# Performance work log

Hardware: AMD Instinct MI355X
Metric: run time of the kernel (lower is better)

Reference implementation:

```python
import jax, jax.numpy as jnp
import numpy as np

N_NODES = 100000
DEG = 16
N_EDGES = N_NODES * DEG
R = 8          # num_relations
C_IN = 64
C_OUT = 64


def setup_inputs() -> dict:
    key = jax.random.key(0)
    k1, k2, k3, k4 = jax.random.split(key, 4)
    x_feat = jax.random.normal(k1, (N_NODES, C_IN), dtype=jnp.float32)
    # xavier-ish scale for weight
    scale = (6.0 / (C_IN + C_OUT)) ** 0.5
    weight = jax.random.uniform(k2, (R + 1, C_IN, C_OUT), dtype=jnp.float32,
                                minval=-scale, maxval=scale)
    bias = jnp.zeros((C_OUT,), dtype=jnp.float32)
    # fixed-degree CSR: row_ptr = arange * DEG
    csr_row_ptr = (jnp.arange(N_NODES + 1, dtype=jnp.int64) * DEG)
    csr_col_ind = jax.random.randint(k3, (N_EDGES,), 0, N_NODES, dtype=jnp.int64)
    edge_type = jax.random.randint(k4, (N_EDGES,), 0, R, dtype=jnp.int64)
    return {"x_feat": x_feat, "weight": weight, "bias": bias,
            "csr_row_ptr": csr_row_ptr, "csr_col_ind": csr_col_ind,
            "edge_type": edge_type, "dup_count": DEG}


def reference(x_feat, weight, bias, csr_row_ptr, csr_col_ind, edge_type, dup_count):
    n_dst = csr_row_ptr.shape[0] - 1
    n_edges = csr_col_ind.shape[0]
    # per-edge destination node ids from CSR row pointer
    degrees = jnp.diff(csr_row_ptr)
    dst = jnp.repeat(jnp.arange(n_dst, dtype=csr_row_ptr.dtype), degrees,
                     total_repeat_length=n_edges)
    # segment id = (dst, relation) pair
    seg = (dst * R + edge_type).astype(jnp.int32)
    gathered = x_feat[csr_col_ind]                                  # [E, C_in]
    sums = jax.ops.segment_sum(gathered, seg, num_segments=n_dst * R)  # [N*R, C_in]
    counts = jax.ops.segment_sum(jnp.ones((n_edges,), x_feat.dtype), seg,
                                 num_segments=n_dst * R)
    # mean aggregation per (node, relation); empty relations -> 0
    agg = sums / jnp.maximum(counts, 1.0)[:, None]
    agg = agg.reshape(n_dst, R * x_feat.shape[1])                   # [N, R*C_in]
    # root (self) feature appended last, matching weight[-1]
    x_agg = jnp.concatenate([agg, x_feat[:n_dst]], axis=1)          # [N, (R+1)*C_in]
    y = x_agg @ weight.reshape(-1, weight.shape[-1]) + bias         # [N, C_out]
    return y
```

## Files before the change

kernel.cpp:

```cpp
#include <hip/hip_runtime.h>
#include <hip/hip_bf16.h>

#define R_REL   8
#define C_DIM   64
#define K_DIM   576
#define KT_N    18
#define CT_N    4
#define TILE_M  16
#define K_PAD   584

typedef __attribute__((ext_vector_type(8))) short bf16x8;
typedef __attribute__((ext_vector_type(4))) float f32x4;
typedef __attribute__((ext_vector_type(2))) unsigned u32x2;


static __device__ __forceinline__ unsigned short f2bf(float f) {
    union { float f; unsigned u; } v; v.f = f;
    unsigned r = v.u + 0x7FFFu + ((v.u >> 16) & 1u);
    return (unsigned short)(r >> 16);
}
static __device__ __forceinline__ float bf2f(unsigned u16) {
    union { unsigned u; float f; } v; v.u = u16 << 16;
    return v.f;
}

__global__ void pack_w_kernel(const float* __restrict__ w, unsigned int* __restrict__ wf) {
    int t = blockIdx.x * blockDim.x + threadIdx.x;
    if (t >= KT_N * CT_N * 64) return;
    int lane = t & 63;
    int ct   = (t >> 6) & 3;
    int kt   = t >> 8;
    int row0 = kt * 32 + (lane >> 4) * 8;
    int col  = ct * 16 + (lane & 15);
    unsigned short v[8];
#pragma unroll
    for (int j = 0; j < 8; ++j) {
        int rk = row0 + j;
        int wr = (rk < 512) ? rk : 512 + ((rk - 512) & 3) * 16 + ((rk - 512) >> 2);
        v[j] = f2bf(w[wr * C_DIM + col]);
    }
    uint4 o;
    o.x = (unsigned)v[0] | ((unsigned)v[1] << 16);
    o.y = (unsigned)v[2] | ((unsigned)v[3] << 16);
    o.z = (unsigned)v[4] | ((unsigned)v[5] << 16);
    o.w = (unsigned)v[6] | ((unsigned)v[7] << 16);
    ((uint4*)wf)[t] = o;
}

__global__ void cvt_x_kernel(const float* __restrict__ x, unsigned short* __restrict__ xb,
                             int total) {
    int t = blockIdx.x * blockDim.x + threadIdx.x;
    if (t >= total) return;
    int n = t >> 4, c = t & 15;
    const float* xr = x + (size_t)n * C_DIM + c;
    ushort4 o;
    o.x = f2bf(xr[0]);
    o.y = f2bf(xr[16]);
    o.z = f2bf(xr[32]);
    o.w = f2bf(xr[48]);
    *(ushort4*)(xb + (size_t)n * C_DIM + c * 4) = o;
}

#define ACCUM_SWITCH(RELV, VV)                                  \
    switch (RELV) {                                             \
        case 0: s0 += (VV); ++c0; break;                        \
        case 1: s1 += (VV); ++c1; break;                        \
        case 2: s2 += (VV); ++c2; break;                        \
        case 3: s3 += (VV); ++c3; break;                        \
        case 4: s4 += (VV); ++c4; break;                        \
        case 5: s5 += (VV); ++c5; break;                        \
        case 6: s6 += (VV); ++c6; break;                        \
        default: s7 += (VV); ++c7; break;                       \
    }

template<int USE_BF>
__global__ __launch_bounds__(256, 8) void rgcn_kernel(
    const float* __restrict__ x_feat,
    const unsigned short* __restrict__ xb,
    const float* __restrict__ bias,
    const int*   __restrict__ row_ptr,
    const int*   __restrict__ col_ind,
    const int*   __restrict__ edge_type,
    const unsigned short* __restrict__ wfrag,
    float* __restrict__ out,
    int n_nodes)
{
    __shared__ __align__(16) unsigned short xa[TILE_M][K_PAD];
    __shared__ __align__(16) int            col_lds[4][64];
    __shared__ __align__(8)  unsigned char  rel_lds[4][64];
    __shared__ __align__(4)  unsigned short inv_lds[4][32];

    const int tid   = threadIdx.x;
    const int lane  = tid & 63;
    const int w     = tid >> 6;
    const int m0    = blockIdx.x * TILE_M;
    const int nbase = m0 + w * 4;

    const int n_l   = nbase + (lane >> 4);
    const bool v_l  = n_l < n_nodes;
    int rp0   = v_l ? row_ptr[n_l]     : 0;
    int rp1   = v_l ? row_ptr[n_l + 1] : 0;
    int deg_l = v_l ? (rp1 - rp0) : -1;
    int col_l = col_ind[rp0 + (lane & 15)];
    int rel_l = edge_type[rp0 + (lane & 15)];

    const bool fast = USE_BF && (__ballot(deg_l == 16) == ~0ull);

    if (fast) {
        col_lds[w][lane] = col_l;
        rel_lds[w][lane] = (unsigned char)rel_l;
        unsigned long long bsel = 0;
#pragma unroll
        for (int r = 0; r < 8; ++r) {
            unsigned long long b = __ballot(rel_l == r);
            bsel = ((lane & 7) == r) ? b : bsel;
        }
        if (lane < 32) {
            int nd  = (lane >> 3) & 3;
            int cnt = __popcll(bsel & (0xFFFFull << (nd * 16)));
            inv_lds[w][lane] = f2bf(1.0f / (float)(cnt > 0 ? cnt : 1));
        }

        u32x2 selfv = *(const u32x2*)(xb + (size_t)(nbase + (lane >> 4)) * C_DIM
                                      + (lane & 15) * 4);
        *(u32x2*)&xa[w * 4 + (lane >> 4)][8 * C_DIM + (lane & 15) * 4] = selfv;

        const int q8 = (lane >> 4) * 8;
        int4 c0a = *(const int4*)&col_lds[w][q8];
        int4 c0b = *(const int4*)&col_lds[w][q8 + 4];
        int4 c1a = *(const int4*)&col_lds[w][32 + q8];
        int4 c1b = *(const int4*)&col_lds[w][32 + q8 + 4];
        int src0[8] = {c0a.x, c0a.y, c0a.z, c0a.w, c0b.x, c0b.y, c0b.z, c0b.w};
        int src1[8] = {c1a.x, c1a.y, c1a.z, c1a.w, c1b.x, c1b.y, c1b.z, c1b.w};

        const unsigned short* xbase = xb + (lane & 15) * 4;
        u32x2 gv0[8], gv1[8];
#pragma unroll
        for (int e = 0; e < 8; ++e) {
            gv0[e] = *(const u32x2*)(xbase + (size_t)src0[e] * C_DIM);
            gv1[e] = *(const u32x2*)(xbase + (size_t)src1[e] * C_DIM);
        }

        unsigned bw0[4][4], bw1[4][4];
#pragma unroll
        for (int d = 0; d < 4; ++d) {
            unsigned lx = gv0[2*d].x, hx = gv0[2*d+1].x;
            unsigned ly = gv0[2*d].y, hy = gv0[2*d+1].y;
            bw0[0][d] = (lx & 0xFFFFu) | (hx << 16);
            bw0[1][d] = (lx >> 16)     | (hx & 0xFFFF0000u);
            bw0[2][d] = (ly & 0xFFFFu) | (hy << 16);
            bw0[3][d] = (ly >> 16)     | (hy & 0xFFFF0000u);
            lx = gv1[2*d].x; hx = gv1[2*d+1].x;
            ly = gv1[2*d].y; hy = gv1[2*d+1].y;
            bw1[0][d] = (lx & 0xFFFFu) | (hx << 16);
            bw1[1][d] = (lx >> 16)     | (hx & 0xFFFF0000u);
            bw1[2][d] = (ly & 0xFFFFu) | (hy << 16);
            bw1[3][d] = (ly >> 16)     | (hy & 0xFFFF0000u);
        }

        const unsigned rl    = lane & 7;
        const bool     hi_ok = (lane >> 5) == ((lane & 15) >> 3);
#pragma unroll
        for (int pr = 0; pr < 2; ++pr) {
            const unsigned char* relp = &rel_lds[w][pr * 32 + q8];
            unsigned rlo = *(const unsigned*)relp;
            unsigned rhi = *(const unsigned*)(relp + 4);
            unsigned inv16 = inv_lds[w][(pr * 2 + ((lane & 15) >> 3)) * 8 + (lane & 7)];
            unsigned invg  = hi_ok ? inv16 : 0u;
            unsigned af[4];
#pragma unroll
            for (int d = 0; d < 4; ++d) {
                unsigned wrd = (d < 2) ? rlo : rhi;
                unsigned b0 = (wrd >> ((d & 1) * 16)) & 0xFFu;
                unsigned b1 = (wrd >> ((d & 1) * 16 + 8)) & 0xFFu;
                af[d] = (b0 == rl ? invg : 0u) | ((b1 == rl ? invg : 0u) << 16);
            }
            union { unsigned u[4]; bf16x8 v; } au;
            au.u[0] = af[0]; au.u[1] = af[1]; au.u[2] = af[2]; au.u[3] = af[3];

#pragma unroll
            for (int g = 0; g < 4; ++g) {
                union { unsigned u[4]; bf16x8 v; } bu;
                if (pr == 0) {
                    bu.u[0] = bw0[g][0]; bu.u[1] = bw0[g][1];
                    bu.u[2] = bw0[g][2]; bu.u[3] = bw0[g][3];
                } else {
                    bu.u[0] = bw1[g][0]; bu.u[1] = bw1[g][1];
                    bu.u[2] = bw1[g][2]; bu.u[3] = bw1[g][3];
                }
                f32x4 dacc = __builtin_amdgcn_mfma_f32_16x16x32_bf16(
                                 au.v, bu.v, (f32x4){0.f, 0.f, 0.f, 0.f}, 0, 0, 0);
#pragma unroll
                for (int reg = 0; reg < 4; ++reg) {
                    int m = (lane >> 4) * 4 + reg;
                    xa[w * 4 + pr * 2 + (m >> 3)][(m & 7) * C_DIM + g * 16 + (lane & 15)]
                        = f2bf(dacc[reg]);
                }
            }
        }
    } else {
        for (int mi_ = 0; mi_ < 4; ++mi_) {
            const int mi = w * 4 + mi_;
            const int n  = nbase + mi_;
            const int sdeg  = __builtin_amdgcn_readlane(deg_l, mi_ * 16);
            const int sbase = __builtin_amdgcn_readlane(rp0,   mi_ * 16);
            if (sdeg < 0) {
                for (int k = lane; k < K_DIM; k += 64) xa[mi][k] = 0;
                continue;
            }
            float s0=0,s1=0,s2=0,s3=0,s4=0,s5=0,s6=0,s7=0;
            int   c0=0,c1=0,c2=0,c3=0,c4=0,c5=0,c6=0,c7=0;
            const int ich = (lane & 15) * 4 + (lane >> 4);
            for (int e = 0; e < sdeg; ++e) {
                int src = col_ind[sbase + e];
                int rlv = edge_type[sbase + e];
                float vv = USE_BF ? bf2f(xb[(size_t)src * C_DIM + ich])
                                  : x_feat[(size_t)src * C_DIM + lane];
                ACCUM_SWITCH(rlv, vv)
            }
            xa[mi][0*C_DIM+lane] = f2bf(s0 * __fdividef(1.0f, (float)(c0>0?c0:1)));
            xa[mi][1*C_DIM+lane] = f2bf(s1 * __fdividef(1.0f, (float)(c1>0?c1:1)));
            xa[mi][2*C_DIM+lane] = f2bf(s2 * __fdividef(1.0f, (float)(c2>0?c2:1)));
            xa[mi][3*C_DIM+lane] = f2bf(s3 * __fdividef(1.0f, (float)(c3>0?c3:1)));
            xa[mi][4*C_DIM+lane] = f2bf(s4 * __fdividef(1.0f, (float)(c4>0?c4:1)));
            xa[mi][5*C_DIM+lane] = f2bf(s5 * __fdividef(1.0f, (float)(c5>0?c5:1)));
            xa[mi][6*C_DIM+lane] = f2bf(s6 * __fdividef(1.0f, (float)(c6>0?c6:1)));
            xa[mi][7*C_DIM+lane] = f2bf(s7 * __fdividef(1.0f, (float)(c7>0?c7:1)));
            xa[mi][8*C_DIM+lane] = USE_BF ? (unsigned short)xb[(size_t)n * C_DIM + lane]
                                          : f2bf(x_feat[(size_t)n * C_DIM
                                                        + (lane & 3) * 16 + (lane >> 2)]);
        }
    }
    __syncthreads();

    const int ct   = w;
    f32x4 acc = {0,0,0,0};
    const int arow = lane & 15;
    const int kgrp2 = lane >> 4;
    const bf16x8* wf8 = (const bf16x8*)wfrag;
#pragma unroll
    for (int kt = 0; kt < KT_N; ++kt) {
        bf16x8 a = *(const bf16x8*)&xa[arow][kt * 32 + kgrp2 * 8];
        acc = __builtin_amdgcn_mfma_f32_16x16x32_bf16(a, wf8[(kt*4 + ct)*64 + lane], acc, 0,0,0);
    }

    const int col   = ct * 16 + (lane & 15);
    const float b   = bias[col];
    const int rbase = (lane >> 4) * 4;
#pragma unroll
    for (int j = 0; j < 4; ++j) {
        int n = m0 + rbase + j;
        if (n < n_nodes)
            out[n * C_DIM + col] = acc[j] + b;
    }
}

extern "C" void kernel_launch(void* const* d_in, const int* in_sizes, int n_in,
                              void* d_out, int out_size, void* d_ws, size_t ws_size,
                              hipStream_t stream) {
    const float* x_feat    = (const float*)d_in[0];
    const float* weight    = (const float*)d_in[1];
    const float* bias      = (const float*)d_in[2];
    const int*   row_ptr   = (const int*)d_in[3];
    const int*   col_ind   = (const int*)d_in[4];
    const int*   edge_type = (const int*)d_in[5];
    float* out = (float*)d_out;

    const int n_nodes = in_sizes[3] - 1;
    const int nblocks = (n_nodes + TILE_M - 1) / TILE_M;

    unsigned int* wfrag = (unsigned int*)d_ws;
    const size_t wf_bytes = (size_t)KT_N * CT_N * 64 * 16;
    const size_t xb_bytes = (size_t)n_nodes * C_DIM * 2;

    pack_w_kernel<<<(KT_N * CT_N * 64 + 255) / 256, 256, 0, stream>>>(weight, wfrag);

    if (ws_size >= wf_bytes + xb_bytes) {
        unsigned short* xb = (unsigned short*)((char*)d_ws + wf_bytes);
        int total = n_nodes * 16;
        cvt_x_kernel<<<(total + 255) / 256, 256, 0, stream>>>(x_feat, xb, total);
        rgcn_kernel<1><<<nblocks, 256, 0, stream>>>(x_feat, xb, bias, row_ptr, col_ind,
                                                    edge_type, (const unsigned short*)d_ws,
                                                    out, n_nodes);
    } else {
        rgcn_kernel<0><<<nblocks, 256, 0, stream>>>(x_feat, nullptr, bias, row_ptr, col_ind,
                                                    edge_type, (const unsigned short*)d_ws,
                                                    out, n_nodes);
    }
}
```

Measured before the change: 56.44 us.

## Fuse weight pack and x conversion, use bpermute for columns, pack LDS writes

```diff
diff --git a/kernel.cpp b/kernel.cpp
--- a/kernel.cpp
+++ b/kernel.cpp
@@ -8,6 +8,7 @@
 #define CT_N    4
 #define TILE_M  16
 #define K_PAD   584
+#define PACK_T  (KT_N * CT_N * 64)
 
 typedef __attribute__((ext_vector_type(8))) short bf16x8;
 typedef __attribute__((ext_vector_type(4))) float f32x4;
@@ -24,34 +25,40 @@
     return v.f;
 }
 
-__global__ void pack_w_kernel(const float* __restrict__ w, unsigned int* __restrict__ wf) {
-    int t = blockIdx.x * blockDim.x + threadIdx.x;
-    if (t >= KT_N * CT_N * 64) return;
-    int lane = t & 63;
-    int ct   = (t >> 6) & 3;
-    int kt   = t >> 8;
-    int row0 = kt * 32 + (lane >> 4) * 8;
-    int col  = ct * 16 + (lane & 15);
-    unsigned short v[8];
-#pragma unroll
-    for (int j = 0; j < 8; ++j) {
-        int rk = row0 + j;
-        int wr = (rk < 512) ? rk : 512 + ((rk - 512) & 3) * 16 + ((rk - 512) >> 2);
-        v[j] = f2bf(w[wr * C_DIM + col]);
-    }
-    uint4 o;
-    o.x = (unsigned)v[0] | ((unsigned)v[1] << 16);
-    o.y = (unsigned)v[2] | ((unsigned)v[3] << 16);
-    o.z = (unsigned)v[4] | ((unsigned)v[5] << 16);
-    o.w = (unsigned)v[6] | ((unsigned)v[7] << 16);
-    ((uint4*)wf)[t] = o;
-}
-
-__global__ void cvt_x_kernel(const float* __restrict__ x, unsigned short* __restrict__ xb,
-                             int total) {
-    int t = blockIdx.x * blockDim.x + threadIdx.x;
-    if (t >= total) return;
-    int n = t >> 4, c = t & 15;
+__global__ void prep_kernel(const float* __restrict__ x, const float* __restrict__ wt,
+                            unsigned short* __restrict__ xb, unsigned int* __restrict__ wf,
+                            int total_cvt) {
+    int t = blockIdx.x * 256 + threadIdx.x;
+    if (t < PACK_T) {
+        int lane = t & 63;
+        int ct   = (t >> 6) & 3;
+        int kt   = t >> 8;
+        int row0 = kt * 32 + (lane >> 4) * 8;
+        int col  = ct * 16 + (lane & 15);
+        unsigned short v[8];
+#pragma unroll
+        for (int j = 0; j < 8; ++j) {
+            int rk = row0 + j;
+            int wr;
+            if (rk < 512) {
+                int rel = rk & 7, c = (rk >> 3) & 15, g = rk >> 7;
+                wr = rel * C_DIM + g * 16 + c;
+            } else {
+                wr = 512 + ((rk - 512) & 3) * 16 + ((rk - 512) >> 2);
+            }
+            v[j] = f2bf(wt[wr * C_DIM + col]);
+        }
+        uint4 o;
+        o.x = (unsigned)v[0] | ((unsigned)v[1] << 16);
+        o.y = (unsigned)v[2] | ((unsigned)v[3] << 16);
+        o.z = (unsigned)v[4] | ((unsigned)v[5] << 16);
+        o.w = (unsigned)v[6] | ((unsigned)v[7] << 16);
+        ((uint4*)wf)[t] = o;
+        return;
+    }
+    int tc = t - PACK_T;
+    if (tc >= total_cvt) return;
+    int n = tc >> 4, c = tc & 15;
     const float* xr = x + (size_t)n * C_DIM + c;
     ushort4 o;
     o.x = f2bf(xr[0]);
@@ -86,7 +93,6 @@
     int n_nodes)
 {
     __shared__ __align__(16) unsigned short xa[TILE_M][K_PAD];
-    __shared__ __align__(16) int            col_lds[4][64];
     __shared__ __align__(8)  unsigned char  rel_lds[4][64];
     __shared__ __align__(4)  unsigned short inv_lds[4][32];
 
@@ -107,7 +113,6 @@
     const bool fast = USE_BF && (__ballot(deg_l == 16) == ~0ull);
 
     if (fast) {
-        col_lds[w][lane] = col_l;
         rel_lds[w][lane] = (unsigned char)rel_l;
         unsigned long long bsel = 0;
 #pragma unroll
@@ -125,13 +130,14 @@
                                       + (lane & 15) * 4);
         *(u32x2*)&xa[w * 4 + (lane >> 4)][8 * C_DIM + (lane & 15) * 4] = selfv;
 
-        const int q8 = (lane >> 4) * 8;
-        int4 c0a = *(const int4*)&col_lds[w][q8];
-        int4 c0b = *(const int4*)&col_lds[w][q8 + 4];
-        int4 c1a = *(const int4*)&col_lds[w][32 + q8];
-        int4 c1b = *(const int4*)&col_lds[w][32 + q8 + 4];
-        int src0[8] = {c0a.x, c0a.y, c0a.z, c0a.w, c0b.x, c0b.y, c0b.z, c0b.w};
-        int src1[8] = {c1a.x, c1a.y, c1a.z, c1a.w, c1b.x, c1b.y, c1b.z, c1b.w};
+        const int q   = lane >> 4;
+        const int q8b = q << 5;
+        int src0[8], src1[8];
+#pragma unroll
+        for (int e = 0; e < 8; ++e) {
+            src0[e] = __builtin_amdgcn_ds_bpermute(q8b + e * 4,       col_l);
+            src1[e] = __builtin_amdgcn_ds_bpermute(q8b + 128 + e * 4, col_l);
+        }
 
         const unsigned short* xbase = xb + (lane & 15) * 4;
         u32x2 gv0[8], gv1[8];
@@ -160,9 +166,11 @@
 
         const unsigned rl    = lane & 7;
         const bool     hi_ok = (lane >> 5) == ((lane & 15) >> 3);
+        const int rb   = (q & 1) * 4;
+        const int nrow = q >> 1;
 #pragma unroll
         for (int pr = 0; pr < 2; ++pr) {
-            const unsigned char* relp = &rel_lds[w][pr * 32 + q8];
+            const unsigned char* relp = &rel_lds[w][pr * 32 + q * 8];
             unsigned rlo = *(const unsigned*)relp;
             unsigned rhi = *(const unsigned*)(relp + 4);
             unsigned inv16 = inv_lds[w][(pr * 2 + ((lane & 15) >> 3)) * 8 + (lane & 7)];
@@ -178,6 +186,7 @@
             union { unsigned u[4]; bf16x8 v; } au;
             au.u[0] = af[0]; au.u[1] = af[1]; au.u[2] = af[2]; au.u[3] = af[3];
 
+            unsigned short* xrow = &xa[w * 4 + pr * 2 + nrow][(lane & 15) * 8 + rb];
 #pragma unroll
             for (int g = 0; g < 4; ++g) {
                 union { unsigned u[4]; bf16x8 v; } bu;
@@ -190,12 +199,10 @@
                 }
                 f32x4 dacc = __builtin_amdgcn_mfma_f32_16x16x32_bf16(
                                  au.v, bu.v, (f32x4){0.f, 0.f, 0.f, 0.f}, 0, 0, 0);
-#pragma unroll
-                for (int reg = 0; reg < 4; ++reg) {
-                    int m = (lane >> 4) * 4 + reg;
-                    xa[w * 4 + pr * 2 + (m >> 3)][(m & 7) * C_DIM + g * 16 + (lane & 15)]
-                        = f2bf(dacc[reg]);
-                }
+                unsigned w0p = (unsigned)f2bf(dacc[0]) | ((unsigned)f2bf(dacc[1]) << 16);
+                unsigned w1p = (unsigned)f2bf(dacc[2]) | ((unsigned)f2bf(dacc[3]) << 16);
+                *(unsigned*)(xrow + g * 128)     = w0p;
+                *(unsigned*)(xrow + g * 128 + 2) = w1p;
             }
         }
     } else {
@@ -218,14 +225,15 @@
                                   : x_feat[(size_t)src * C_DIM + lane];
                 ACCUM_SWITCH(rlv, vv)
             }
-            xa[mi][0*C_DIM+lane] = f2bf(s0 * __fdividef(1.0f, (float)(c0>0?c0:1)));
-            xa[mi][1*C_DIM+lane] = f2bf(s1 * __fdividef(1.0f, (float)(c1>0?c1:1)));
-            xa[mi][2*C_DIM+lane] = f2bf(s2 * __fdividef(1.0f, (float)(c2>0?c2:1)));
-            xa[mi][3*C_DIM+lane] = f2bf(s3 * __fdividef(1.0f, (float)(c3>0?c3:1)));
-            xa[mi][4*C_DIM+lane] = f2bf(s4 * __fdividef(1.0f, (float)(c4>0?c4:1)));
-            xa[mi][5*C_DIM+lane] = f2bf(s5 * __fdividef(1.0f, (float)(c5>0?c5:1)));
-            xa[mi][6*C_DIM+lane] = f2bf(s6 * __fdividef(1.0f, (float)(c6>0?c6:1)));
-            xa[mi][7*C_DIM+lane] = f2bf(s7 * __fdividef(1.0f, (float)(c7>0?c7:1)));
+            const int kb = (lane >> 4) * 128 + (lane & 15) * 8;
+            xa[mi][kb + 0] = f2bf(s0 * __fdividef(1.0f, (float)(c0>0?c0:1)));
+            xa[mi][kb + 1] = f2bf(s1 * __fdividef(1.0f, (float)(c1>0?c1:1)));
+            xa[mi][kb + 2] = f2bf(s2 * __fdividef(1.0f, (float)(c2>0?c2:1)));
+            xa[mi][kb + 3] = f2bf(s3 * __fdividef(1.0f, (float)(c3>0?c3:1)));
+            xa[mi][kb + 4] = f2bf(s4 * __fdividef(1.0f, (float)(c4>0?c4:1)));
+            xa[mi][kb + 5] = f2bf(s5 * __fdividef(1.0f, (float)(c5>0?c5:1)));
+            xa[mi][kb + 6] = f2bf(s6 * __fdividef(1.0f, (float)(c6>0?c6:1)));
+            xa[mi][kb + 7] = f2bf(s7 * __fdividef(1.0f, (float)(c7>0?c7:1)));
             xa[mi][8*C_DIM+lane] = USE_BF ? (unsigned short)xb[(size_t)n * C_DIM + lane]
                                           : f2bf(x_feat[(size_t)n * C_DIM
                                                         + (lane & 3) * 16 + (lane >> 2)]);
@@ -270,19 +278,19 @@
     const int nblocks = (n_nodes + TILE_M - 1) / TILE_M;
 
     unsigned int* wfrag = (unsigned int*)d_ws;
-    const size_t wf_bytes = (size_t)KT_N * CT_N * 64 * 16;
+    const size_t wf_bytes = (size_t)PACK_T * 16;
     const size_t xb_bytes = (size_t)n_nodes * C_DIM * 2;
-
-    pack_w_kernel<<<(KT_N * CT_N * 64 + 255) / 256, 256, 0, stream>>>(weight, wfrag);
 
     if (ws_size >= wf_bytes + xb_bytes) {
         unsigned short* xb = (unsigned short*)((char*)d_ws + wf_bytes);
-        int total = n_nodes * 16;
-        cvt_x_kernel<<<(total + 255) / 256, 256, 0, stream>>>(x_feat, xb, total);
+        int total_cvt = n_nodes * 16;
+        int prep_blocks = (PACK_T + total_cvt + 255) / 256;
+        prep_kernel<<<prep_blocks, 256, 0, stream>>>(x_feat, weight, xb, wfrag, total_cvt);
         rgcn_kernel<1><<<nblocks, 256, 0, stream>>>(x_feat, xb, bias, row_ptr, col_ind,
                                                     edge_type, (const unsigned short*)d_ws,
                                                     out, n_nodes);
     } else {
+        prep_kernel<<<(PACK_T + 255) / 256, 256, 0, stream>>>(x_feat, weight, nullptr, wfrag, 0);
         rgcn_kernel<0><<<nblocks, 256, 0, stream>>>(x_feat, nullptr, bias, row_ptr, col_ind,
                                                     edge_type, (const unsigned short*)d_ws,
                                                     out, n_nodes);
```

New measurement: 51.67 us (median of 2 runs). -8.4%, faster.
